# Kernel tuning notes

Measured on AMD Instinct MI355X. Metric: run time of the kernel, lower is better.

## Reference

```python
import jax, jax.numpy as jnp
import numpy as np

# Geometry constants (from config)
H, D_BOT, P, K, D = 4096, 1024, 8, 64, 64
SCALE = 1.0


def setup_inputs() -> dict:
    key = jax.random.key(0)
    ks = jax.random.split(key, 20)
    B, T = 4, 2048

    def lin(k, din, dout, s=0.02):
        kw, kb = jax.random.split(k)
        return (jax.random.normal(kw, (din, dout), jnp.float32) * s,
                jax.random.normal(kb, (dout,), jnp.float32) * s)

    x = jax.random.normal(ks[0], (B, T, H), jnp.float32)
    Wi, bi = lin(ks[1], H, D_BOT)
    Wb, bb = lin(ks[2], D_BOT, P * D)          # base_coord_proj
    Wf, bf = lin(ks[3], D_BOT, P * K)          # fiber_section_proj
    Wl, bl = lin(ks[4], D_BOT, P * (D + K))    # lambda_term_proj
    Ww, bw = lin(ks[5], D_BOT, P)              # mixture_proj_w
    Wm, bm = lin(ks[6], D_BOT, P * D)          # mixture_proj_m
    Ws, bs = lin(ks[7], D_BOT, P * D)          # mixture_proj_s
    Wu, bu = lin(ks[8], D_BOT, P * K)          # mixture_proj_u
    Wo, bo = lin(ks[9], D + K, H)              # output_proj
    return dict(x=x, Wi=Wi, bi=bi, Wb=Wb, bb=bb, Wf=Wf, bf=bf, Wl=Wl, bl=bl,
                Ww=Ww, bw=bw, Wm=Wm, bm=bm, Ws=Ws, bs=bs, Wu=Wu, bu=bu,
                Wo=Wo, bo=bo)


def reference(x, Wi, bi, Wb, bb, Wf, bf, Wl, bl, Ww, bw, Wm, bm, Ws, bs, Wu, bu, Wo, bo):
    B, T, _ = x.shape
    # Shared bottleneck
    h_bot = jnp.einsum('bth,hd->btd', x, Wi) + bi                      # (B,T,D_bot)

    # Fan-out of small parallel projections (fused-QKV-like opportunity)
    base_coords = (jnp.einsum('btd,de->bte', h_bot, Wb) + bb).reshape(B, T, P, D)
    base_coords = jnp.clip(base_coords, -10.0, 10.0)
    fiber_sections = (jnp.einsum('btd,de->bte', h_bot, Wf) + bf).reshape(B, T, P, K)
    lambda_terms = (jnp.einsum('btd,de->bte', h_bot, Wl) + bl).reshape(B, T, P, D + K)
    w_logits = jnp.einsum('btd,dp->btp', h_bot, Ww) + bw               # (B,T,P)
    m = (jnp.einsum('btd,de->bte', h_bot, Wm) + bm).reshape(B, T, P, D)
    log_s = jnp.clip((jnp.einsum('btd,de->bte', h_bot, Ws) + bs).reshape(B, T, P, D), -5.0, 5.0)
    u = (jnp.einsum('btd,de->bte', h_bot, Wu) + bu).reshape(B, T, P, K)

    # Lambda operations / info-geometric update treated as identity (undefined in source)
    updated_sections = fiber_sections

    # Parallel transport correction along the T axis: curr - 0.1*(curr - prev)
    prev = base_coords[:, :-1]
    curr = base_coords[:, 1:]
    transported = jnp.concatenate(
        [base_coords[:, :1], curr - 0.1 * (curr - prev)], axis=1)       # (B,T,P,D)
    updated_coords = transported

    # Mixture aggregation
    weights = jax.nn.softmax(w_logits, axis=-1)                         # (B,T,P)
    agg_coords = jnp.einsum('btp,btpd->btd', weights, updated_coords)   # (B,T,D)
    agg_sections = jnp.einsum('btp,btpk->btk', weights, updated_sections)  # (B,T,K)

    combined = jnp.concatenate([agg_coords, agg_sections], axis=-1)     # (B,T,D+K)
    output = jnp.einsum('bte,eh->bth', combined, Wo) + bo               # (B,T,H)
    return x + SCALE * output
```

## Files before the change

kernel.cpp:

```cpp
#include <hip/hip_runtime.h>
#include <hip/hip_bf16.h>
#include <stdint.h>

typedef __hip_bfloat16 bf16;
typedef __attribute__((ext_vector_type(8))) short short8;
typedef __attribute__((ext_vector_type(4))) short short4_t;
typedef __attribute__((ext_vector_type(4))) float float4_t;

__device__ __forceinline__ short f2b_bits(float f) {
  union { float f; unsigned u; } v; v.f = f;
  unsigned r = (v.u + 0x7FFF + ((v.u >> 16) & 1)) >> 16;
  return (short)r;
}
__device__ __forceinline__ bf16 f2b(float f) {
  short s = f2b_bits(f);
  bf16 h; __builtin_memcpy(&h, &s, 2);
  return h;
}
__device__ __forceinline__ bf16 ld_bf16(const void* p, size_t idx, int f32) {
  if (f32) return f2b(((const float*)p)[idx]);
  return ((const bf16*)p)[idx];
}

__device__ __forceinline__ void gload_lds16(const void* g, void* l) {
  __builtin_amdgcn_global_load_lds(
      (const __attribute__((address_space(1))) void*)g,
      (__attribute__((address_space(3))) void*)l, 16, 0, 0);
}

__global__ void detect_dtype(const void* probe, int* flag) {
  int lane = threadIdx.x;
  const unsigned short* u = (const unsigned short*)probe;
  const float* fp = (const float*)probe;
  int cb = 0, cf = 0;
  for (int j = lane; j < 256; j += 64) {
    unsigned short he = u[2 * j];
    int e = (he >> 7) & 0xFF;
    cb += (e >= 0x60 && e <= 0x7E);
    float af = fabsf(fp[j]);
    cf += (af > 1e-9f && af < 1.0f);
  }
#pragma unroll
  for (int off = 32; off > 0; off >>= 1) {
    cb += __shfl_down(cb, off);
    cf += __shfl_down(cf, off);
  }
  if (lane == 0) *flag = (cf > cb) ? 1 : 0;
}

__global__ __launch_bounds__(256) void transpose_all(
    const void* __restrict__ Wi, const void* __restrict__ Wb,
    const void* __restrict__ Wf, const void* __restrict__ Wo,
    bf16* __restrict__ WiT, bf16* __restrict__ WbfT2, bf16* __restrict__ WoT,
    const int* __restrict__ flagp)
{
  const int f32 = *flagp;
  int b = blockIdx.x;
  const void* src; bf16* dst; int K, N, tb;
  if (b < 1024)      { src = Wi; dst = WiT;              K = 4096; N = 1024; tb = b; }
  else if (b < 1152) { src = Wb; dst = WbfT2;            K = 1024; N = 512;  tb = b - 1024; }
  else if (b < 1280) { src = Wf; dst = WbfT2 + 512*1024; K = 1024; N = 512;  tb = b - 1152; }
  else               { src = Wo; dst = WoT;              K = 128;  N = 4096; tb = b - 1280; }
  int nbk = K >> 6;
  int kb = (tb % nbk) * 64, nb = (tb / nbk) * 64;
  __shared__ bf16 tile[64][65];
  int tx = threadIdx.x & 63;
  int ty = threadIdx.x >> 6;
#pragma unroll
  for (int i = 0; i < 64; i += 4)
    tile[ty + i][tx] = ld_bf16(src, (size_t)(kb + ty + i) * N + nb + tx, f32);
  __syncthreads();
#pragma unroll
  for (int i = 0; i < 64; i += 4)
    dst[(size_t)(nb + ty + i) * K + kb + tx] = tile[tx][ty + i];
}

__global__ __launch_bounds__(256) void cvt_small(
    const void* __restrict__ Ww, const void* __restrict__ bw,
    const void* __restrict__ bi, const void* __restrict__ bb,
    const void* __restrict__ bf_, const void* __restrict__ bo,
    bf16* __restrict__ WbfT2, bf16* __restrict__ bbf2,
    bf16* __restrict__ biC, bf16* __restrict__ boC,
    const int* __restrict__ flagp)
{
  const int f32 = *flagp;
  int i = blockIdx.x * 256 + threadIdx.x;
  if (i < 131072) {
    int r = i >> 10, k = i & 1023;
    bf16 v = (r < 8) ? ld_bf16(Ww, (size_t)k * 8 + r, f32) : f2b(0.f);
    WbfT2[(size_t)(1024 + r) * 1024 + k] = v;
  }
  if (i < 128) bbf2[1024 + i] = (i < 8) ? ld_bf16(bw, i, f32) : f2b(0.f);
  if (i < 1024) biC[i] = ld_bf16(bi, i, f32);
  if (i < 512)  bbf2[i] = ld_bf16(bb, i, f32);
  if (i < 512)  bbf2[512 + i] = ld_bf16(bf_, i, f32);
  if (i < 4096) boC[i] = ld_bf16(bo, i, f32);
}

template <int BM, int BN>
__device__ __forceinline__ void gemm_core(
    const void* __restrict__ A,
    const bf16* __restrict__ BT,
    const bf16* __restrict__ bias,
    const void* __restrict__ resid,
    void* __restrict__ C,
    const int* __restrict__ aF32, const int* __restrict__ rF32,
    const int* __restrict__ cF32,
    int M, int N, int K, int clip_cols)
{
  static_assert(BM == 64 && BN == 128, "epilogue assumes 64x128");
  constexpr int FM = BM / 32;
  constexpr int FN = BN / 32;
  __shared__ alignas(16) char smem[(BM + BN) * 64 * 2];
  bf16* As = (bf16*)smem;
  bf16* Bs = (bf16*)smem + BM * 64;
  const int af32 = aF32 ? *aF32 : 0;
  const int rf32 = rF32 ? *rF32 : 0;
  const int cf32 = cF32 ? *cF32 : 0;
  const int tid  = threadIdx.x;
  const int wave = tid >> 6;
  const int lane = tid & 63;
  const int m0 = blockIdx.x * BM;
  const int n0 = blockIdx.y * BN;
  const int wm = (wave >> 1) * (BM / 2);
  const int wn = (wave & 1) * (BN / 2);
  const int lm = lane & 15;
  const int lk = (lane >> 4) * 8;

  float4_t acc[FM][FN];
#pragma unroll
  for (int i = 0; i < FM; i++)
#pragma unroll
    for (int j = 0; j < FN; j++) acc[i][j] = (float4_t){0.f, 0.f, 0.f, 0.f};

  for (int k0 = 0; k0 < K; k0 += 64) {
#pragma unroll
    for (int i = 0; i < BN / 32; i++) {
      int V = tid + 256 * i;
      int row = V >> 3;
      int kc  = (V & 7) * 8;
      gload_lds16(BT + (size_t)(n0 + row) * K + k0 + kc, Bs + (size_t)V * 8);
    }
#pragma unroll
    for (int i = 0; i < BM / 32; i++) {
      int V = tid + 256 * i;
      int row = V >> 3;
      int kc  = (V & 7) * 8;
      if (af32) {
        const float* ap = (const float*)A + (size_t)(m0 + row) * K + k0 + kc;
        float4_t f0 = *(const float4_t*)ap;
        float4_t f1 = *(const float4_t*)(ap + 4);
        short8 v;
        v[0] = f2b_bits(f0[0]); v[1] = f2b_bits(f0[1]);
        v[2] = f2b_bits(f0[2]); v[3] = f2b_bits(f0[3]);
        v[4] = f2b_bits(f1[0]); v[5] = f2b_bits(f1[1]);
        v[6] = f2b_bits(f1[2]); v[7] = f2b_bits(f1[3]);
        *(short8*)(As + (size_t)V * 8) = v;
      } else {
        gload_lds16((const bf16*)A + (size_t)(m0 + row) * K + k0 + kc,
                    As + (size_t)V * 8);
      }
    }
    __syncthreads();
#pragma unroll
    for (int kk = 0; kk < 64; kk += 32) {
      short8 af[FM], bfr[FN];
#pragma unroll
      for (int mi = 0; mi < FM; mi++)
        af[mi] = *(const short8*)(As + (wm + mi * 16 + lm) * 64 + kk + lk);
#pragma unroll
      for (int ni = 0; ni < FN; ni++)
        bfr[ni] = *(const short8*)(Bs + (wn + ni * 16 + lm) * 64 + kk + lk);
#pragma unroll
      for (int mi = 0; mi < FM; mi++)
#pragma unroll
        for (int ni = 0; ni < FN; ni++)
          acc[mi][ni] = __builtin_amdgcn_mfma_f32_16x16x32_bf16(
              af[mi], bfr[ni], acc[mi][ni], 0, 0, 0);
    }
    __syncthreads();
  }

  float* EP = (float*)smem;
  const int ep_c = (tid & 15) * 4;
#pragma unroll
  for (int h = 0; h < 2; h++) {
    if ((wn >> 6) == h) {
#pragma unroll
      for (int mi = 0; mi < FM; mi++)
#pragma unroll
        for (int ni = 0; ni < FN; ni++) {
          int cl = (wn - h * 64) + ni * 16 + lm;
#pragma unroll
          for (int r = 0; r < 4; r++) {
            int rw = wm + mi * 16 + (lane >> 4) * 4 + r;
            EP[rw * 68 + cl] = acc[mi][ni][r];
          }
        }
    }
    __syncthreads();
#pragma unroll
    for (int i = 0; i < 4; i++) {
      int rw  = (tid >> 4) + 16 * i;
      int gr  = m0 + rw;
      int col = n0 + h * 64 + ep_c;
      size_t idx = (size_t)gr * N + col;
      float4_t v = *(const float4_t*)(EP + rw * 68 + ep_c);
      float o[4];
#pragma unroll
      for (int j = 0; j < 4; j++) {
        float t = v[j] + __bfloat162float(bias[col + j]);
        if (col + j < clip_cols) t = fminf(fmaxf(t, -10.f), 10.f);
        o[j] = t;
      }
      if (resid) {
        if (rf32) {
          float4_t rv = *(const float4_t*)((const float*)resid + idx);
#pragma unroll
          for (int j = 0; j < 4; j++) o[j] += rv[j];
        } else {
          short4_t rv = *(const short4_t*)((const bf16*)resid + idx);
#pragma unroll
          for (int j = 0; j < 4; j++) {
            bf16 hb; short sb = rv[j]; __builtin_memcpy(&hb, &sb, 2);
            o[j] += __bfloat162float(hb);
          }
        }
      }
      if (cf32) {
        *(float4_t*)((float*)C + idx) = (float4_t){o[0], o[1], o[2], o[3]};
      } else {
        short4_t pv;
#pragma unroll
        for (int j = 0; j < 4; j++) pv[j] = f2b_bits(o[j]);
        *(short4_t*)((bf16*)C + idx) = pv;
      }
    }
    __syncthreads();
  }
}

__global__ __launch_bounds__(256) void gemm_x(
    const void* A, const bf16* BT, const bf16* bias, const void* resid,
    void* C, const int* aF32, const int* rF32, const int* cF32,
    int M, int N, int K, int clip_cols) {
  gemm_core<64, 128>(A, BT, bias, resid, C, aF32, rF32, cF32, M, N, K, clip_cols);
}
__global__ __launch_bounds__(256) void gemm_h(
    const void* A, const bf16* BT, const bf16* bias, const void* resid,
    void* C, const int* aF32, const int* rF32, const int* cF32,
    int M, int N, int K, int clip_cols) {
  gemm_core<64, 128>(A, BT, bias, resid, C, aF32, rF32, cF32, M, N, K, clip_cols);
}
__global__ __launch_bounds__(256) void gemm_o(
    const void* A, const bf16* BT, const bf16* bias, const void* resid,
    void* C, const int* aF32, const int* rF32, const int* cF32,
    int M, int N, int K, int clip_cols) {
  gemm_core<64, 128>(A, BT, bias, resid, C, aF32, rF32, cF32, M, N, K, clip_cols);
}

__global__ __launch_bounds__(128) void build_combined(
    const bf16* __restrict__ bcfs,
    bf16* __restrict__ comb)
{
  int t = blockIdx.x;
  int tid = threadIdx.x;
  int tl = t & 2047;
  __shared__ float lg[8];
  __shared__ float w[8];
  if (tid < 8) lg[tid] = __bfloat162float(bcfs[(size_t)t * 1152 + 1024 + tid]);
  __syncthreads();
  if (tid < 8) {
    float mx = lg[0];
#pragma unroll
    for (int i = 1; i < 8; i++) mx = fmaxf(mx, lg[i]);
    float den = 0.f;
#pragma unroll
    for (int i = 0; i < 8; i++) den += expf(lg[i] - mx);
    w[tid] = expf(lg[tid] - mx) / den;
  }
  __syncthreads();
  float s = 0.f;
  if (tid < 64) {
    int d = tid;
    const bf16* bc = bcfs + (size_t)t * 1152;
    size_t tp = (tl == 0) ? (size_t)t : (size_t)t - 1;
    const bf16* bp = bcfs + tp * 1152;
#pragma unroll
    for (int p = 0; p < 8; p++) {
      float cur = __bfloat162float(bc[p * 64 + d]);
      float v = (tl == 0) ? cur : (0.9f * cur + 0.1f * __bfloat162float(bp[p * 64 + d]));
      s += w[p] * v;
    }
  } else {
    int d = tid - 64;
    const bf16* fsrow = bcfs + (size_t)t * 1152 + 512;
#pragma unroll
    for (int p = 0; p < 8; p++) s += w[p] * __bfloat162float(fsrow[p * 64 + d]);
  }
  comb[(size_t)t * 128 + tid] = __float2bfloat16(s);
}

extern "C" void kernel_launch(void* const* d_in, const int* in_sizes, int n_in,
                              void* d_out, int out_size, void* d_ws, size_t ws_size,
                              hipStream_t stream) {
  (void)in_sizes; (void)n_in; (void)out_size; (void)ws_size;
  const void* x   = d_in[0];
  const void* Wi  = d_in[1];
  const void* bi  = d_in[2];
  const void* Wb  = d_in[3];
  const void* bb  = d_in[4];
  const void* Wf  = d_in[5];
  const void* bfv = d_in[6];
  const void* Ww  = d_in[9];
  const void* bw  = d_in[10];
  const void* Wo  = d_in[17];
  const void* bo  = d_in[18];

  char* ws = (char*)d_ws;
  bf16*  h_bot = (bf16*)(ws + 0);
  bf16*  comb  = (bf16*)(ws + 0);
  bf16*  bcfs  = (bf16*)(ws + 16777216);
  bf16*  WiT   = (bf16*)(ws + 35651584);
  bf16*  WbfT2 = (bf16*)(ws + 44040192);
  bf16*  WoT   = (bf16*)(ws + 46399488);
  bf16*  biC   = (bf16*)(ws + 47448064);
  bf16*  bbf2C = (bf16*)(ws + 47450112);
  bf16*  boC   = (bf16*)(ws + 47452416);
  int*   flag  = (int*)(ws + 47460608);

  detect_dtype<<<1, 64, 0, stream>>>(bi, flag);

  transpose_all<<<1408, 256, 0, stream>>>(Wi, Wb, Wf, Wo, WiT, WbfT2, WoT, flag);
  cvt_small<<<512, 256, 0, stream>>>(Ww, bw, bi, bb, bfv, bo,
                                     WbfT2, bbf2C, biC, boC, flag);

  gemm_x<<<dim3(128, 8), 256, 0, stream>>>(
      x, WiT, biC, nullptr, h_bot, flag, nullptr, nullptr,
      8192, 1024, 4096, 0);
  gemm_h<<<dim3(128, 9), 256, 0, stream>>>(
      h_bot, WbfT2, bbf2C, nullptr, bcfs, nullptr, nullptr, nullptr,
      8192, 1152, 1024, 512);
  build_combined<<<8192, 128, 0, stream>>>(bcfs, comb);
  gemm_o<<<dim3(128, 32), 256, 0, stream>>>(
      comb, WoT, boC, x, d_out, nullptr, flag, flag,
      8192, 4096, 128, 0);
}
```

Before: 507.6 us.

## Pre-convert x to bf16 and double-buffer LDS in GEMMs with async loads

Adds a pass that converts the fp32 input x to bf16 in workspace (when the workspace is large enough), so the first GEMM can use direct global-to-LDS loads instead of converting inline. The GEMM core gains a double-buffered LDS pipeline that prefetches the next K tile while MFMAs run on the current one, synchronised with vmcnt waits and raw barriers. This targets load latency in the main GEMMs. The price is an extra read and write of x in the conversion pass and twice the LDS per block, which may lower occupancy.

```diff
diff --git a/kernel.cpp b/kernel.cpp
--- a/kernel.cpp
+++ b/kernel.cpp
@@ -46,6 +46,30 @@
     cf += __shfl_down(cf, off);
   }
   if (lane == 0) *flag = (cf > cb) ? 1 : 0;
+}
+
+__global__ __launch_bounds__(256) void cvt_x(const void* __restrict__ x,
+                                             bf16* __restrict__ xb,
+                                             const int* __restrict__ flagp,
+                                             size_t n) {
+  const int f32 = *flagp;
+  size_t i = ((size_t)blockIdx.x * 256 + threadIdx.x) * 8;
+  size_t stride = (size_t)gridDim.x * 256 * 8;
+  for (; i < n; i += stride) {
+    if (f32) {
+      const float* xp = (const float*)x + i;
+      float4_t f0 = *(const float4_t*)xp;
+      float4_t f1 = *(const float4_t*)(xp + 4);
+      short8 v;
+      v[0] = f2b_bits(f0[0]); v[1] = f2b_bits(f0[1]);
+      v[2] = f2b_bits(f0[2]); v[3] = f2b_bits(f0[3]);
+      v[4] = f2b_bits(f1[0]); v[5] = f2b_bits(f1[1]);
+      v[6] = f2b_bits(f1[2]); v[7] = f2b_bits(f1[3]);
+      *(short8*)(xb + i) = v;
+    } else {
+      *(short8*)(xb + i) = *(const short8*)((const bf16*)x + i);
+    }
+  }
 }
 
 __global__ __launch_bounds__(256) void transpose_all(
@@ -97,20 +121,164 @@
   if (i < 4096) boC[i] = ld_bf16(bo, i, f32);
 }
 
-template <int BM, int BN>
-__device__ __forceinline__ void gemm_core(
-    const void* __restrict__ A,
+__device__ __forceinline__ void epilogue_64x128(
+    char* smem, float4_t (&acc)[2][4], const bf16* bias, const void* resid,
+    void* C, int rf32, int cf32, int m0, int n0, int N, int clip_cols,
+    int tid, int lane, int wm, int wn, int lm)
+{
+  float* EP = (float*)smem;
+  const int ep_c = (tid & 15) * 4;
+#pragma unroll
+  for (int h = 0; h < 2; h++) {
+    if ((wn >> 6) == h) {
+#pragma unroll
+      for (int mi = 0; mi < 2; mi++)
+#pragma unroll
+        for (int ni = 0; ni < 4; ni++) {
+          int cl = (wn - h * 64) + ni * 16 + lm;
+#pragma unroll
+          for (int r = 0; r < 4; r++) {
+            int rw = wm + mi * 16 + (lane >> 4) * 4 + r;
+            EP[rw * 68 + cl] = acc[mi][ni][r];
+          }
+        }
+    }
+    __syncthreads();
+#pragma unroll
+    for (int i = 0; i < 4; i++) {
+      int rw  = (tid >> 4) + 16 * i;
+      int gr  = m0 + rw;
+      int col = n0 + h * 64 + ep_c;
+      size_t idx = (size_t)gr * N + col;
+      float4_t v = *(const float4_t*)(EP + rw * 68 + ep_c);
+      float o[4];
+#pragma unroll
+      for (int j = 0; j < 4; j++) {
+        float t = v[j] + __bfloat162float(bias[col + j]);
+        if (col + j < clip_cols) t = fminf(fmaxf(t, -10.f), 10.f);
+        o[j] = t;
+      }
+      if (resid) {
+        if (rf32) {
+          float4_t rv = *(const float4_t*)((const float*)resid + idx);
+#pragma unroll
+          for (int j = 0; j < 4; j++) o[j] += rv[j];
+        } else {
+          short4_t rv = *(const short4_t*)((const bf16*)resid + idx);
+#pragma unroll
+          for (int j = 0; j < 4; j++) {
+            bf16 hb; short sb = rv[j]; __builtin_memcpy(&hb, &sb, 2);
+            o[j] += __bfloat162float(hb);
+          }
+        }
+      }
+      if (cf32) {
+        *(float4_t*)((float*)C + idx) = (float4_t){o[0], o[1], o[2], o[3]};
+      } else {
+        short4_t pv;
+#pragma unroll
+        for (int j = 0; j < 4; j++) pv[j] = f2b_bits(o[j]);
+        *(short4_t*)((bf16*)C + idx) = pv;
+      }
+    }
+    __syncthreads();
+  }
+}
+
+__device__ __forceinline__ void gemm_core_db(
+    const bf16* __restrict__ A,
     const bf16* __restrict__ BT,
     const bf16* __restrict__ bias,
     const void* __restrict__ resid,
     void* __restrict__ C,
-    const int* __restrict__ aF32, const int* __restrict__ rF32,
-    const int* __restrict__ cF32,
+    const int* __restrict__ rF32, const int* __restrict__ cF32,
     int M, int N, int K, int clip_cols)
 {
-  static_assert(BM == 64 && BN == 128, "epilogue assumes 64x128");
-  constexpr int FM = BM / 32;
-  constexpr int FN = BN / 32;
+  constexpr int BM = 64, BN = 128;
+  __shared__ alignas(16) char smem[2 * (BM + BN) * 64 * 2];
+  bf16* As0 = (bf16*)smem;
+  bf16* As1 = (bf16*)(smem + 16384 / 2);
+  bf16* Bs0 = (bf16*)(smem + 16384);
+  bf16* Bs1 = (bf16*)(smem + 16384 + 16384);
+  const int rf32 = rF32 ? *rF32 : 0;
+  const int cf32 = cF32 ? *cF32 : 0;
+  const int tid  = threadIdx.x;
+  const int wave = tid >> 6;
+  const int lane = tid & 63;
+  const int m0 = blockIdx.x * BM;
+  const int n0 = blockIdx.y * BN;
+  const int wm = (wave >> 1) * (BM / 2);
+  const int wn = (wave & 1) * (BN / 2);
+  const int lm = lane & 15;
+  const int lk = (lane >> 4) * 8;
+
+  auto stage = [&](bf16* as, bf16* bs, int k0) {
+#pragma unroll
+    for (int i = 0; i < BN / 32; i++) {
+      int V = tid + 256 * i;
+      gload_lds16(BT + (size_t)(n0 + (V >> 3)) * K + k0 + (V & 7) * 8,
+                  bs + (size_t)V * 8);
+    }
+#pragma unroll
+    for (int i = 0; i < BM / 32; i++) {
+      int V = tid + 256 * i;
+      gload_lds16(A + (size_t)(m0 + (V >> 3)) * K + k0 + (V & 7) * 8,
+                  as + (size_t)V * 8);
+    }
+  };
+
+  float4_t acc[2][4];
+#pragma unroll
+  for (int i = 0; i < 2; i++)
+#pragma unroll
+    for (int j = 0; j < 4; j++) acc[i][j] = (float4_t){0.f, 0.f, 0.f, 0.f};
+
+  const int NT = K >> 6;
+  stage(As0, Bs0, 0);
+
+  for (int t = 0; t < NT; t++) {
+    bf16* Asc = (t & 1) ? As1 : As0;
+    bf16* Bsc = (t & 1) ? Bs1 : Bs0;
+    if (t + 1 < NT) {
+      stage((t & 1) ? As0 : As1, (t & 1) ? Bs0 : Bs1, (t + 1) << 6);
+      asm volatile("s_waitcnt vmcnt(6)" ::: "memory");
+    } else {
+      asm volatile("s_waitcnt vmcnt(0)" ::: "memory");
+    }
+    __builtin_amdgcn_sched_barrier(0);
+    __builtin_amdgcn_s_barrier();
+    __builtin_amdgcn_sched_barrier(0);
+#pragma unroll
+    for (int kk = 0; kk < 64; kk += 32) {
+      short8 af[2], bfr[4];
+#pragma unroll
+      for (int mi = 0; mi < 2; mi++)
+        af[mi] = *(const short8*)(Asc + (wm + mi * 16 + lm) * 64 + kk + lk);
+#pragma unroll
+      for (int ni = 0; ni < 4; ni++)
+        bfr[ni] = *(const short8*)(Bsc + (wn + ni * 16 + lm) * 64 + kk + lk);
+#pragma unroll
+      for (int mi = 0; mi < 2; mi++)
+#pragma unroll
+        for (int ni = 0; ni < 4; ni++)
+          acc[mi][ni] = __builtin_amdgcn_mfma_f32_16x16x32_bf16(
+              af[mi], bfr[ni], acc[mi][ni], 0, 0, 0);
+    }
+    __builtin_amdgcn_sched_barrier(0);
+    __builtin_amdgcn_s_barrier();
+  }
+  epilogue_64x128(smem, acc, bias, resid, C, rf32, cf32,
+                  m0, n0, N, clip_cols, tid, lane, wm, wn, lm);
+}
+
+__device__ __forceinline__ void gemm_core_sb(
+    const void* __restrict__ A, const bf16* __restrict__ BT,
+    const bf16* __restrict__ bias, const void* __restrict__ resid,
+    void* __restrict__ C, const int* __restrict__ aF32,
+    const int* __restrict__ rF32, const int* __restrict__ cF32,
+    int M, int N, int K, int clip_cols)
+{
+  constexpr int BM = 64, BN = 128;
   __shared__ alignas(16) char smem[(BM + BN) * 64 * 2];
   bf16* As = (bf16*)smem;
   bf16* Bs = (bf16*)smem + BM * 64;
@@ -127,25 +295,23 @@
   const int lm = lane & 15;
   const int lk = (lane >> 4) * 8;
 
-  float4_t acc[FM][FN];
-#pragma unroll
-  for (int i = 0; i < FM; i++)
-#pragma unroll
-    for (int j = 0; j < FN; j++) acc[i][j] = (float4_t){0.f, 0.f, 0.f, 0.f};
+  float4_t acc[2][4];
+#pragma unroll
+  for (int i = 0; i < 2; i++)
+#pragma unroll
+    for (int j = 0; j < 4; j++) acc[i][j] = (float4_t){0.f, 0.f, 0.f, 0.f};
 
   for (int k0 = 0; k0 < K; k0 += 64) {
 #pragma unroll
     for (int i = 0; i < BN / 32; i++) {
       int V = tid + 256 * i;
-      int row = V >> 3;
-      int kc  = (V & 7) * 8;
-      gload_lds16(BT + (size_t)(n0 + row) * K + k0 + kc, Bs + (size_t)V * 8);
+      gload_lds16(BT + (size_t)(n0 + (V >> 3)) * K + k0 + (V & 7) * 8,
+                  Bs + (size_t)V * 8);
     }
 #pragma unroll
     for (int i = 0; i < BM / 32; i++) {
       int V = tid + 256 * i;
-      int row = V >> 3;
-      int kc  = (V & 7) * 8;
+      int row = V >> 3, kc = (V & 7) * 8;
       if (af32) {
         const float* ap = (const float*)A + (size_t)(m0 + row) * K + k0 + kc;
         float4_t f0 = *(const float4_t*)ap;
@@ -164,99 +330,46 @@
     __syncthreads();
 #pragma unroll
     for (int kk = 0; kk < 64; kk += 32) {
-      short8 af[FM], bfr[FN];
-#pragma unroll
-      for (int mi = 0; mi < FM; mi++)
+      short8 af[2], bfr[4];
+#pragma unroll
+      for (int mi = 0; mi < 2; mi++)
         af[mi] = *(const short8*)(As + (wm + mi * 16 + lm) * 64 + kk + lk);
 #pragma unroll
-      for (int ni = 0; ni < FN; ni++)
+      for (int ni = 0; ni < 4; ni++)
         bfr[ni] = *(const short8*)(Bs + (wn + ni * 16 + lm) * 64 + kk + lk);
 #pragma unroll
-      for (int mi = 0; mi < FM; mi++)
-#pragma unroll
-        for (int ni = 0; ni < FN; ni++)
+      for (int mi = 0; mi < 2; mi++)
+#pragma unroll
+        for (int ni = 0; ni < 4; ni++)
           acc[mi][ni] = __builtin_amdgcn_mfma_f32_16x16x32_bf16(
               af[mi], bfr[ni], acc[mi][ni], 0, 0, 0);
     }
     __syncthreads();
   }
-
-  float* EP = (float*)smem;
-  const int ep_c = (tid & 15) * 4;
-#pragma unroll
-  for (int h = 0; h < 2; h++) {
-    if ((wn >> 6) == h) {
-#pragma unroll
-      for (int mi = 0; mi < FM; mi++)
-#pragma unroll
-        for (int ni = 0; ni < FN; ni++) {
-          int cl = (wn - h * 64) + ni * 16 + lm;
-#pragma unroll
-          for (int r = 0; r < 4; r++) {
-            int rw = wm + mi * 16 + (lane >> 4) * 4 + r;
-            EP[rw * 68 + cl] = acc[mi][ni][r];
-          }
-        }
-    }
-    __syncthreads();
-#pragma unroll
-    for (int i = 0; i < 4; i++) {
-      int rw  = (tid >> 4) + 16 * i;
-      int gr  = m0 + rw;
-      int col = n0 + h * 64 + ep_c;
-      size_t idx = (size_t)gr * N + col;
-      float4_t v = *(const float4_t*)(EP + rw * 68 + ep_c);
-      float o[4];
-#pragma unroll
-      for (int j = 0; j < 4; j++) {
-        float t = v[j] + __bfloat162float(bias[col + j]);
-        if (col + j < clip_cols) t = fminf(fmaxf(t, -10.f), 10.f);
-        o[j] = t;
-      }
-      if (resid) {
-        if (rf32) {
-          float4_t rv = *(const float4_t*)((const float*)resid + idx);
-#pragma unroll
-          for (int j = 0; j < 4; j++) o[j] += rv[j];
-        } else {
-          short4_t rv = *(const short4_t*)((const bf16*)resid + idx);
-#pragma unroll
-          for (int j = 0; j < 4; j++) {
-            bf16 hb; short sb = rv[j]; __builtin_memcpy(&hb, &sb, 2);
-            o[j] += __bfloat162float(hb);
-          }
-        }
-      }
-      if (cf32) {
-        *(float4_t*)((float*)C + idx) = (float4_t){o[0], o[1], o[2], o[3]};
-      } else {
-        short4_t pv;
-#pragma unroll
-        for (int j = 0; j < 4; j++) pv[j] = f2b_bits(o[j]);
-        *(short4_t*)((bf16*)C + idx) = pv;
-      }
-    }
-    __syncthreads();
-  }
+  epilogue_64x128(smem, acc, bias, resid, C, rf32, cf32,
+                  m0, n0, N, clip_cols, tid, lane, wm, wn, lm);
 }
 
 __global__ __launch_bounds__(256) void gemm_x(
+    const bf16* A, const bf16* BT, const bf16* bias, const void* resid,
+    void* C, const int* rF32, const int* cF32, int M, int N, int K, int clip_cols) {
+  gemm_core_db(A, BT, bias, resid, C, rF32, cF32, M, N, K, clip_cols);
+}
+__global__ __launch_bounds__(256) void gemm_x_f(
     const void* A, const bf16* BT, const bf16* bias, const void* resid,
     void* C, const int* aF32, const int* rF32, const int* cF32,
     int M, int N, int K, int clip_cols) {
-  gemm_core<64, 128>(A, BT, bias, resid, C, aF32, rF32, cF32, M, N, K, clip_cols);
+  gemm_core_sb(A, BT, bias, resid, C, aF32, rF32, cF32, M, N, K, clip_cols);
 }
 __global__ __launch_bounds__(256) void gemm_h(
-    const void* A, const bf16* BT, const bf16* bias, const void* resid,
-    void* C, const int* aF32, const int* rF32, const int* cF32,
-    int M, int N, int K, int clip_cols) {
-  gemm_core<64, 128>(A, BT, bias, resid, C, aF32, rF32, cF32, M, N, K, clip_cols);
+    const bf16* A, const bf16* BT, const bf16* bias, const void* resid,
+    void* C, const int* rF32, const int* cF32, int M, int N, int K, int clip_cols) {
+  gemm_core_db(A, BT, bias, resid, C, rF32, cF32, M, N, K, clip_cols);
 }
 __global__ __launch_bounds__(256) void gemm_o(
-    const void* A, const bf16* BT, const bf16* bias, const void* resid,
-    void* C, const int* aF32, const int* rF32, const int* cF32,
-    int M, int N, int K, int clip_cols) {
-  gemm_core<64, 128>(A, BT, bias, resid, C, aF32, rF32, cF32, M, N, K, clip_cols);
+    const bf16* A, const bf16* BT, const bf16* bias, const void* resid,
+    void* C, const int* rF32, const int* cF32, int M, int N, int K, int clip_cols) {
+  gemm_core_db(A, BT, bias, resid, C, rF32, cF32, M, N, K, clip_cols);
 }
 
 __global__ __launch_bounds__(128) void build_combined(
@@ -304,7 +417,7 @@
 extern "C" void kernel_launch(void* const* d_in, const int* in_sizes, int n_in,
                               void* d_out, int out_size, void* d_ws, size_t ws_size,
                               hipStream_t stream) {
-  (void)in_sizes; (void)n_in; (void)out_size; (void)ws_size;
+  (void)in_sizes; (void)n_in; (void)out_size;
   const void* x   = d_in[0];
   const void* Wi  = d_in[1];
   const void* bi  = d_in[2];
@@ -328,21 +441,31 @@
   bf16*  bbf2C = (bf16*)(ws + 47450112);
   bf16*  boC   = (bf16*)(ws + 47452416);
   int*   flag  = (int*)(ws + 47460608);
+  bf16*  xb    = (bf16*)(ws + 47464448);
+  const bool use_xb = ws_size >= (size_t)47464448 + 67108864;
 
   detect_dtype<<<1, 64, 0, stream>>>(bi, flag);
+
+  if (use_xb)
+    cvt_x<<<2048, 256, 0, stream>>>(x, xb, flag, (size_t)8192 * 4096);
 
   transpose_all<<<1408, 256, 0, stream>>>(Wi, Wb, Wf, Wo, WiT, WbfT2, WoT, flag);
   cvt_small<<<512, 256, 0, stream>>>(Ww, bw, bi, bb, bfv, bo,
                                      WbfT2, bbf2C, biC, boC, flag);
 
-  gemm_x<<<dim3(128, 8), 256, 0, stream>>>(
-      x, WiT, biC, nullptr, h_bot, flag, nullptr, nullptr,
-      8192, 1024, 4096, 0);
+  if (use_xb)
+    gemm_x<<<dim3(128, 8), 256, 0, stream>>>(
+        xb, WiT, biC, nullptr, h_bot, nullptr, nullptr,
+        8192, 1024, 4096, 0);
+  else
+    gemm_x_f<<<dim3(128, 8), 256, 0, stream>>>(
+        x, WiT, biC, nullptr, h_bot, flag, nullptr, nullptr,
+        8192, 1024, 4096, 0);
   gemm_h<<<dim3(128, 9), 256, 0, stream>>>(
-      h_bot, WbfT2, bbf2C, nullptr, bcfs, nullptr, nullptr, nullptr,
+      h_bot, WbfT2, bbf2C, nullptr, bcfs, nullptr, nullptr,
       8192, 1152, 1024, 512);
   build_combined<<<8192, 128, 0, stream>>>(bcfs, comb);
   gemm_o<<<dim3(128, 32), 256, 0, stream>>>(
-      comb, WoT, boC, x, d_out, nullptr, flag, flag,
+      comb, WoT, boC, x, d_out, flag, flag,
       8192, 4096, 128, 0);
 }
```

New measurement: 528.2 us. 4.1% more time.
